# Kernel tuning notes

Measured on AMD Instinct MI355X. Metric: run time of the kernel, lower is better.

The kernel has to match this reference:

```python
import jax, jax.numpy as jnp
import numpy as np

B, T, C = 4, 2048, 2048
N_HEAD = 16
HEAD_DIM = C // N_HEAD  # 128


def _apply_rotary_emb(x, cos, sin):
    # x: (B, T, H, D), cos/sin: (1, T, 1, D/2)
    d = x.shape[-1] // 2
    x1, x2 = x[..., :d], x[..., d:]
    return jnp.concatenate([x1 * cos + x2 * sin, -x2 * sin + x1 * cos], axis=-1)


def setup_inputs() -> dict:
    key = jax.random.key(0)
    ks = jax.random.split(key, 7)
    s = 0.02
    return {
        "x": jax.random.normal(ks[0], (B, T, C), dtype=jnp.float32),
        "cos": jax.random.normal(ks[1], (1, T, 1, HEAD_DIM // 2), dtype=jnp.float32),
        "sin": jax.random.normal(ks[2], (1, T, 1, HEAD_DIM // 2), dtype=jnp.float32),
        "wq": jax.random.normal(ks[3], (C, C), dtype=jnp.float32) * s,
        "wk": jax.random.normal(ks[4], (C, C), dtype=jnp.float32) * s,
        "wv": jax.random.normal(ks[5], (C, C), dtype=jnp.float32) * s,
        "wo": jax.random.normal(ks[6], (C, C), dtype=jnp.float32) * s,
    }


def reference(x, cos, sin, wq, wk, wv, wo):
    b, t, c = x.shape
    h, d = N_HEAD, HEAD_DIM
    # linear projections (torch Linear: x @ W.T), reshape to (B, T, H, D)
    q = (x @ wq.T).reshape(b, t, h, d)
    k = (x @ wk.T).reshape(b, t, h, d)
    v = (x @ wv.T).reshape(b, t, h, d)
    q = _apply_rotary_emb(q, cos, sin)
    k = _apply_rotary_emb(k, cos, sin)
    # scaled dot-product attention, non-causal; heads on axis 2
    scale = 1.0 / jnp.sqrt(jnp.float32(d))
    scores = jnp.einsum("bqhd,bkhd->bhqk", q, k) * scale
    attn = jax.nn.softmax(scores, axis=-1)
    y = jnp.einsum("bhqk,bkhd->bqhd", attn, v).reshape(b, t, c)
    return y @ wo.T
```

## Files before the change

### kernel.cpp

```cpp
#include <hip/hip_runtime.h>

#define B_SZ 4
#define T_SZ 2048
#define C_SZ 2048
#define H_SZ 16
#define D_SZ 128

typedef __attribute__((ext_vector_type(8))) __bf16 bf16x8;
typedef __attribute__((ext_vector_type(4))) float f32x4;
typedef __attribute__((ext_vector_type(4))) unsigned short us4;

static __device__ __forceinline__ unsigned short f2bf(float f) {
  unsigned u = __builtin_bit_cast(unsigned, f);
  u += 0x7fffu + ((u >> 16) & 1u);
  return (unsigned short)(u >> 16);
}

static __device__ __forceinline__ void gload16(const void* g, void* l) {
  __builtin_amdgcn_global_load_lds((__attribute__((address_space(1))) void*)(g),
                                   (__attribute__((address_space(3))) void*)(l), 16, 0, 0);
}

__global__ __launch_bounds__(256) void cast_f32_bf16(const float* __restrict__ src,
                                                     unsigned short* __restrict__ dst, int n4) {
  int i = blockIdx.x * 256 + threadIdx.x;
  if (i >= n4) return;
  float4 v = ((const float4*)src)[i];
  us4 o;
  o[0] = f2bf(v.x); o[1] = f2bf(v.y); o[2] = f2bf(v.z); o[3] = f2bf(v.w);
  ((us4*)dst)[i] = o;
}

template <int EPI>
__global__ __launch_bounds__(256) void gemm_bt(const unsigned short* __restrict__ A,
                                               const unsigned short* __restrict__ W,
                                               void* __restrict__ out,
                                               const float* __restrict__ cosp,
                                               const float* __restrict__ sinp,
                                               float outScale, int M, int N, int K) {
  __shared__ unsigned short As[128 * 32];
  __shared__ unsigned short Bs[128 * 32];
  const int tid = threadIdx.x;
  const int wave = tid >> 6, lane = tid & 63, quad = lane >> 4, l15 = lane & 15;
  const int m0 = blockIdx.y * 128, n0 = blockIdx.x * 128;
  f32x4 acc[2][8] = {};
  for (int kt = 0; kt < K; kt += 32) {
    __syncthreads();
#pragma unroll
    for (int s = 0; s < 2; ++s) {
      int i = s * 256 + tid;
      int row = i >> 2, pos = i & 3, c = pos ^ (row & 3);
      gload16(A + (size_t)(m0 + row) * K + kt + c * 8, (char*)As + i * 16);
      gload16(W + (size_t)(n0 + row) * K + kt + c * 8, (char*)Bs + i * 16);
    }
    __syncthreads();
    const int sw = (quad ^ (l15 & 3)) * 8;
    bf16x8 a0 = *(const bf16x8*)&As[(wave * 32 + l15) * 32 + sw];
    bf16x8 a1 = *(const bf16x8*)&As[(wave * 32 + 16 + l15) * 32 + sw];
#pragma unroll
    for (int nt = 0; nt < 8; ++nt) {
      bf16x8 b = *(const bf16x8*)&Bs[(nt * 16 + l15) * 32 + sw];
      acc[0][nt] = __builtin_amdgcn_mfma_f32_16x16x32_bf16(a0, b, acc[0][nt], 0, 0, 0);
      acc[1][nt] = __builtin_amdgcn_mfma_f32_16x16x32_bf16(a1, b, acc[1][nt], 0, 0, 0);
    }
  }
  const int mb = m0 + wave * 32;
  if (EPI == 1) {
    unsigned short* O = (unsigned short*)out;
#pragma unroll
    for (int mt = 0; mt < 2; ++mt)
#pragma unroll
      for (int r = 0; r < 4; ++r) {
        int m = mb + mt * 16 + quad * 4 + r;
        int t = m & (T_SZ - 1);
#pragma unroll
        for (int nt = 0; nt < 4; ++nt) {
          int dd = nt * 16 + l15;
          float c = cosp[t * 64 + dd];
          float s = sinp[t * 64 + dd];
          float x1 = acc[mt][nt][r], x2 = acc[mt][nt + 4][r];
          O[(size_t)m * N + n0 + dd]      = f2bf((x1 * c + x2 * s) * outScale);
          O[(size_t)m * N + n0 + dd + 64] = f2bf((x1 * c - x2 * s) * outScale);
        }
      }
  } else if (EPI == 2) {
    unsigned short* O = (unsigned short*)out;
#pragma unroll
    for (int mt = 0; mt < 2; ++mt) {
      int m4 = mb + mt * 16 + quad * 4;
      int bb = m4 >> 11;
      int t = m4 & (T_SZ - 1);
#pragma unroll
      for (int nt = 0; nt < 8; ++nt) {
        int n = n0 + nt * 16 + l15;
        int h = n >> 7, d = n & (D_SZ - 1);
        us4 pk;
        pk[0] = f2bf(acc[mt][nt][0]);
        pk[1] = f2bf(acc[mt][nt][1]);
        pk[2] = f2bf(acc[mt][nt][2]);
        pk[3] = f2bf(acc[mt][nt][3]);
        *(us4*)&O[((size_t)((bb * H_SZ + h) * D_SZ + d)) * T_SZ + t] = pk;
      }
    }
  } else {
    float* O = (float*)out;
#pragma unroll
    for (int mt = 0; mt < 2; ++mt)
#pragma unroll
      for (int nt = 0; nt < 8; ++nt)
#pragma unroll
        for (int r = 0; r < 4; ++r) {
          int m = mb + mt * 16 + quad * 4 + r;
          O[(size_t)m * N + n0 + nt * 16 + l15] = acc[mt][nt][r];
        }
  }
}

__global__ __launch_bounds__(256, 2) void attn_fused(const unsigned short* __restrict__ Q,
                                                     const unsigned short* __restrict__ Kg,
                                                     const unsigned short* __restrict__ Vt,
                                                     unsigned short* __restrict__ Y) {
  __shared__ unsigned short Ks[2][64 * 128];
  __shared__ unsigned short Vs[2][128 * 64];
  __shared__ unsigned short Ps[4][32 * 40];
  const int tid = threadIdx.x;
  const int wave = tid >> 6, lane = tid & 63, quad = lane >> 4, l15 = lane & 15;
  const int kh = wave & 1, qh = wave >> 1;
  const int qt = blockIdx.x, bh = blockIdx.y;
  const int b = bh >> 4, h = bh & 15;
  const float LOG2E = 1.44269504088896f;

  bf16x8 aq[2][4];
  {
    size_t qrow0 = (size_t)(b * T_SZ + qt * 64 + qh * 32);
#pragma unroll
    for (int nt = 0; nt < 2; ++nt)
#pragma unroll
      for (int ks = 0; ks < 4; ++ks)
        aq[nt][ks] = *(const bf16x8*)(Q + (qrow0 + nt * 16 + l15) * C_SZ + h * D_SZ + ks * 32 + quad * 8);
  }

  const size_t kbase0 = ((size_t)(b * T_SZ)) * C_SZ + h * D_SZ;
  const size_t vbase0 = ((size_t)(bh * D_SZ)) * T_SZ;
#pragma unroll
  for (int s = 0; s < 4; ++s) {
    int ii = s * 256 + tid;
    int krow = ii >> 4, kpos = ii & 15, kc = kpos ^ (krow & 15);
    gload16(Kg + kbase0 + (size_t)krow * C_SZ + kc * 8, (char*)Ks[0] + ii * 16);
    int vrow = ii >> 3, vpos = ii & 7, vc = vpos ^ (vrow & 7);
    gload16(Vt + vbase0 + (size_t)vrow * T_SZ + vc * 8, (char*)Vs[0] + ii * 16);
  }
  float mstate[2] = {-1e30f, -1e30f}, lstate[2] = {0.f, 0.f};
  f32x4 o[8][2] = {};
  unsigned short* PsW = Ps[wave];
  __syncthreads();

  for (int kt = 0; kt < T_SZ / 64; ++kt) {
    const int cur = kt & 1;
    bf16x8 bk[2][4];
#pragma unroll
    for (int mt = 0; mt < 2; ++mt)
#pragma unroll
      for (int ks = 0; ks < 4; ++ks)
        bk[mt][ks] = *(const bf16x8*)&Ks[cur][(kh * 32 + mt * 16 + l15) * 128 + (((ks * 4 + quad) ^ l15) * 8)];
    bf16x8 bv[8];
#pragma unroll
    for (int dt = 0; dt < 8; ++dt)
      bv[dt] = *(const bf16x8*)&Vs[cur][(dt * 16 + l15) * 64 + (((kh * 4 + quad) ^ (l15 & 7)) * 8)];
    if (kt + 1 < T_SZ / 64) {
      const int nxt = cur ^ 1;
      size_t kb = kbase0 + (size_t)(kt + 1) * 64 * C_SZ;
      size_t vb = vbase0 + (size_t)(kt + 1) * 64;
#pragma unroll
      for (int s = 0; s < 4; ++s) {
        int ii = s * 256 + tid;
        int krow = ii >> 4, kpos = ii & 15, kc = kpos ^ (krow & 15);
        gload16(Kg + kb + (size_t)krow * C_SZ + kc * 8, (char*)Ks[nxt] + ii * 16);
        int vrow = ii >> 3, vpos = ii & 7, vc = vpos ^ (vrow & 7);
        gload16(Vt + vb + (size_t)vrow * T_SZ + vc * 8, (char*)Vs[nxt] + ii * 16);
      }
    }
    f32x4 sf[2][2] = {};
#pragma unroll
    for (int mt = 0; mt < 2; ++mt)
#pragma unroll
      for (int ks = 0; ks < 4; ++ks)
#pragma unroll
        for (int nt = 0; nt < 2; ++nt)
          sf[mt][nt] = __builtin_amdgcn_mfma_f32_16x16x32_bf16(bk[mt][ks], aq[nt][ks], sf[mt][nt], 0, 0, 0);
    float alpha[2];
#pragma unroll
    for (int nt = 0; nt < 2; ++nt) {
      float rmax = sf[0][nt][0];
#pragma unroll
      for (int mt = 0; mt < 2; ++mt)
#pragma unroll
        for (int r = 0; r < 4; ++r) rmax = fmaxf(rmax, sf[mt][nt][r]);
      rmax = fmaxf(rmax, __shfl_xor(rmax, 16));
      rmax = fmaxf(rmax, __shfl_xor(rmax, 32));
      float mnew = fmaxf(mstate[nt], rmax);
      alpha[nt] = exp2f((mstate[nt] - mnew) * LOG2E);
      float rsum = 0.f;
#pragma unroll
      for (int mt = 0; mt < 2; ++mt) {
        us4 pk;
#pragma unroll
        for (int r = 0; r < 4; ++r) {
          float p = exp2f((sf[mt][nt][r] - mnew) * LOG2E);
          rsum += p;
          pk[r] = f2bf(p);
        }
        *(us4*)&PsW[(nt * 16 + l15) * 40 + mt * 16 + quad * 4] = pk;
      }
      rsum += __shfl_xor(rsum, 16);
      rsum += __shfl_xor(rsum, 32);
      lstate[nt] = lstate[nt] * alpha[nt] + rsum;
      mstate[nt] = mnew;
    }
#pragma unroll
    for (int dt = 0; dt < 8; ++dt)
#pragma unroll
      for (int nt = 0; nt < 2; ++nt)
#pragma unroll
        for (int r = 0; r < 4; ++r) o[dt][nt][r] *= alpha[nt];
    bf16x8 ap[2];
#pragma unroll
    for (int nt = 0; nt < 2; ++nt)
      ap[nt] = *(const bf16x8*)&PsW[(nt * 16 + l15) * 40 + quad * 8];
#pragma unroll
    for (int dt = 0; dt < 8; ++dt)
#pragma unroll
      for (int nt = 0; nt < 2; ++nt)
        o[dt][nt] = __builtin_amdgcn_mfma_f32_16x16x32_bf16(bv[dt], ap[nt], o[dt][nt], 0, 0, 0);
    __syncthreads();
  }

  float* Xch = (float*)Ks;
  float* st  = (float*)Vs;
  if (kh == 1) {
#pragma unroll
    for (int dt = 0; dt < 8; ++dt)
#pragma unroll
      for (int nt = 0; nt < 2; ++nt)
        *(f32x4*)&Xch[((qh * 16 + dt * 2 + nt) * 64 + lane) * 4] = o[dt][nt];
    if (quad == 0) {
#pragma unroll
      for (int nt = 0; nt < 2; ++nt) {
        int q = qh * 32 + nt * 16 + l15;
        st[q] = mstate[nt];
        st[64 + q] = lstate[nt];
      }
    }
  }
  __syncthreads();
  if (kh == 0) {
#pragma unroll
    for (int nt = 0; nt < 2; ++nt) {
      int q = qh * 32 + nt * 16 + l15;
      float m1 = st[q], l1 = st[64 + q];
      float M = fmaxf(mstate[nt], m1);
      float a0 = exp2f((mstate[nt] - M) * LOG2E);
      float a1 = exp2f((m1 - M) * LOG2E);
      float L = lstate[nt] * a0 + l1 * a1;
      float inv = 1.0f / L;
      size_t row = (size_t)(b * T_SZ + qt * 64) + q;
#pragma unroll
      for (int dt = 0; dt < 8; ++dt) {
        f32x4 o1 = *(const f32x4*)&Xch[((qh * 16 + dt * 2 + nt) * 64 + lane) * 4];
        us4 pk;
#pragma unroll
        for (int r = 0; r < 4; ++r)
          pk[r] = f2bf((o[dt][nt][r] * a0 + o1[r] * a1) * inv);
        *(us4*)&Y[row * C_SZ + h * D_SZ + dt * 16 + quad * 4] = pk;
      }
    }
  }
}

extern "C" void kernel_launch(void* const* d_in, const int* in_sizes, int n_in,
                              void* d_out, int out_size, void* d_ws, size_t ws_size,
                              hipStream_t stream) {
  (void)in_sizes; (void)n_in; (void)out_size; (void)ws_size;
  const float* x    = (const float*)d_in[0];
  const float* cosp = (const float*)d_in[1];
  const float* sinp = (const float*)d_in[2];
  const float* wq   = (const float*)d_in[3];
  const float* wk   = (const float*)d_in[4];
  const float* wv   = (const float*)d_in[5];
  const float* wo   = (const float*)d_in[6];
  float* out = (float*)d_out;

  const size_t XE = (size_t)B_SZ * T_SZ * C_SZ;
  const size_t WE = (size_t)C_SZ * C_SZ;
  unsigned short* Xb = (unsigned short*)d_ws;
  unsigned short* Qb = Xb + XE;
  unsigned short* Kb = Qb + XE;
  unsigned short* Vt = Kb + XE;
  unsigned short* Wb = Vt + XE;
  unsigned short* Y  = Xb;

  const int M = B_SZ * T_SZ, N = C_SZ, K = C_SZ;
  dim3 ggrid(N / 128, M / 128);
  int nbx = (int)(XE / 4 / 256);
  int nbw = (int)(WE / 4 / 256);
  const float qscale = 0.088388347648318447f;

  cast_f32_bf16<<<nbx, 256, 0, stream>>>(x, Xb, (int)(XE / 4));

  cast_f32_bf16<<<nbw, 256, 0, stream>>>(wq, Wb, (int)(WE / 4));
  gemm_bt<1><<<ggrid, 256, 0, stream>>>(Xb, Wb, Qb, cosp, sinp, qscale, M, N, K);

  cast_f32_bf16<<<nbw, 256, 0, stream>>>(wk, Wb, (int)(WE / 4));
  gemm_bt<1><<<ggrid, 256, 0, stream>>>(Xb, Wb, Kb, cosp, sinp, 1.0f, M, N, K);

  cast_f32_bf16<<<nbw, 256, 0, stream>>>(wv, Wb, (int)(WE / 4));
  gemm_bt<2><<<ggrid, 256, 0, stream>>>(Xb, Wb, Vt, nullptr, nullptr, 1.0f, M, N, K);

  attn_fused<<<dim3(T_SZ / 64, B_SZ * H_SZ), 256, 0, stream>>>(Qb, Kb, Vt, Y);

  cast_f32_bf16<<<nbw, 256, 0, stream>>>(wo, Wb, (int)(WE / 4));
  gemm_bt<3><<<ggrid, 256, 0, stream>>>(Y, Wb, out, nullptr, nullptr, 1.0f, M, N, K);
}
```

Baseline: 871.9 us.

## Process two KV tiles per iteration with a single shared online-softmax rescale

The attention loop now handles two 64-key tiles per iteration. It computes both score blocks, takes one running max over 128 keys, and rescales the output accumulator once per pair instead of once per tile. Refills of each LDS buffer are issued as soon as that buffer has been read, behind a barrier, instead of prefetching one tile ahead. This halves the rescale and max-reduction overhead and moves the barriers around. In exchange it raises register pressure (two sets of K/V fragments and score tiles held live), which could hurt occupancy at the launch bound of 2 blocks.

```diff
diff --git a/kernel.cpp b/kernel.cpp
--- a/kernel.cpp
+++ b/kernel.cpp
@@ -116,6 +116,22 @@
   }
 }
 
+static __device__ __forceinline__ void stage_kv(const unsigned short* __restrict__ Kg,
+                                                const unsigned short* __restrict__ Vt,
+                                                unsigned short* Kbuf, unsigned short* Vbuf,
+                                                size_t kbase0, size_t vbase0, int kt, int tid) {
+  size_t kb = kbase0 + (size_t)kt * 64 * C_SZ;
+  size_t vb = vbase0 + (size_t)kt * 64;
+#pragma unroll
+  for (int s = 0; s < 4; ++s) {
+    int ii = s * 256 + tid;
+    int krow = ii >> 4, kpos = ii & 15, kc = kpos ^ (krow & 15);
+    gload16(Kg + kb + (size_t)krow * C_SZ + kc * 8, (char*)Kbuf + ii * 16);
+    int vrow = ii >> 3, vpos = ii & 7, vc = vpos ^ (vrow & 7);
+    gload16(Vt + vb + (size_t)vrow * T_SZ + vc * 8, (char*)Vbuf + ii * 16);
+  }
+}
+
 __global__ __launch_bounds__(256, 2) void attn_fused(const unsigned short* __restrict__ Q,
                                                      const unsigned short* __restrict__ Kg,
                                                      const unsigned short* __restrict__ Vt,
@@ -142,97 +158,131 @@
 
   const size_t kbase0 = ((size_t)(b * T_SZ)) * C_SZ + h * D_SZ;
   const size_t vbase0 = ((size_t)(bh * D_SZ)) * T_SZ;
-#pragma unroll
-  for (int s = 0; s < 4; ++s) {
-    int ii = s * 256 + tid;
-    int krow = ii >> 4, kpos = ii & 15, kc = kpos ^ (krow & 15);
-    gload16(Kg + kbase0 + (size_t)krow * C_SZ + kc * 8, (char*)Ks[0] + ii * 16);
-    int vrow = ii >> 3, vpos = ii & 7, vc = vpos ^ (vrow & 7);
-    gload16(Vt + vbase0 + (size_t)vrow * T_SZ + vc * 8, (char*)Vs[0] + ii * 16);
-  }
+  stage_kv(Kg, Vt, Ks[0], Vs[0], kbase0, vbase0, 0, tid);
+  stage_kv(Kg, Vt, Ks[1], Vs[1], kbase0, vbase0, 1, tid);
+
   float mstate[2] = {-1e30f, -1e30f}, lstate[2] = {0.f, 0.f};
   f32x4 o[8][2] = {};
   unsigned short* PsW = Ps[wave];
   __syncthreads();
 
-  for (int kt = 0; kt < T_SZ / 64; ++kt) {
-    const int cur = kt & 1;
-    bf16x8 bk[2][4];
-#pragma unroll
-    for (int mt = 0; mt < 2; ++mt)
-#pragma unroll
-      for (int ks = 0; ks < 4; ++ks)
-        bk[mt][ks] = *(const bf16x8*)&Ks[cur][(kh * 32 + mt * 16 + l15) * 128 + (((ks * 4 + quad) ^ l15) * 8)];
-    bf16x8 bv[8];
+  for (int jt = 0; jt < T_SZ / 128; ++jt) {
+    bf16x8 bkA[2][4], bvA[8];
+#pragma unroll
+    for (int mt = 0; mt < 2; ++mt)
+#pragma unroll
+      for (int ks = 0; ks < 4; ++ks)
+        bkA[mt][ks] = *(const bf16x8*)&Ks[0][(kh * 32 + mt * 16 + l15) * 128 + (((ks * 4 + quad) ^ l15) * 8)];
 #pragma unroll
     for (int dt = 0; dt < 8; ++dt)
-      bv[dt] = *(const bf16x8*)&Vs[cur][(dt * 16 + l15) * 64 + (((kh * 4 + quad) ^ (l15 & 7)) * 8)];
-    if (kt + 1 < T_SZ / 64) {
-      const int nxt = cur ^ 1;
-      size_t kb = kbase0 + (size_t)(kt + 1) * 64 * C_SZ;
-      size_t vb = vbase0 + (size_t)(kt + 1) * 64;
-#pragma unroll
-      for (int s = 0; s < 4; ++s) {
-        int ii = s * 256 + tid;
-        int krow = ii >> 4, kpos = ii & 15, kc = kpos ^ (krow & 15);
-        gload16(Kg + kb + (size_t)krow * C_SZ + kc * 8, (char*)Ks[nxt] + ii * 16);
-        int vrow = ii >> 3, vpos = ii & 7, vc = vpos ^ (vrow & 7);
-        gload16(Vt + vb + (size_t)vrow * T_SZ + vc * 8, (char*)Vs[nxt] + ii * 16);
-      }
-    }
-    f32x4 sf[2][2] = {};
+      bvA[dt] = *(const bf16x8*)&Vs[0][(dt * 16 + l15) * 64 + (((kh * 4 + quad) ^ (l15 & 7)) * 8)];
+    f32x4 sfA[2][2] = {};
 #pragma unroll
     for (int mt = 0; mt < 2; ++mt)
 #pragma unroll
       for (int ks = 0; ks < 4; ++ks)
 #pragma unroll
         for (int nt = 0; nt < 2; ++nt)
-          sf[mt][nt] = __builtin_amdgcn_mfma_f32_16x16x32_bf16(bk[mt][ks], aq[nt][ks], sf[mt][nt], 0, 0, 0);
-    float alpha[2];
+          sfA[mt][nt] = __builtin_amdgcn_mfma_f32_16x16x32_bf16(bkA[mt][ks], aq[nt][ks], sfA[mt][nt], 0, 0, 0);
+    __syncthreads();
+    if (jt + 1 < T_SZ / 128) stage_kv(Kg, Vt, Ks[0], Vs[0], kbase0, vbase0, 2 * jt + 2, tid);
+    bf16x8 bkB[2][4], bvB[8];
+#pragma unroll
+    for (int mt = 0; mt < 2; ++mt)
+#pragma unroll
+      for (int ks = 0; ks < 4; ++ks)
+        bkB[mt][ks] = *(const bf16x8*)&Ks[1][(kh * 32 + mt * 16 + l15) * 128 + (((ks * 4 + quad) ^ l15) * 8)];
+#pragma unroll
+    for (int dt = 0; dt < 8; ++dt)
+      bvB[dt] = *(const bf16x8*)&Vs[1][(dt * 16 + l15) * 64 + (((kh * 4 + quad) ^ (l15 & 7)) * 8)];
+    f32x4 sfB[2][2] = {};
+#pragma unroll
+    for (int mt = 0; mt < 2; ++mt)
+#pragma unroll
+      for (int ks = 0; ks < 4; ++ks)
+#pragma unroll
+        for (int nt = 0; nt < 2; ++nt)
+          sfB[mt][nt] = __builtin_amdgcn_mfma_f32_16x16x32_bf16(bkB[mt][ks], aq[nt][ks], sfB[mt][nt], 0, 0, 0);
+    float alpha[2], rsum[2];
 #pragma unroll
     for (int nt = 0; nt < 2; ++nt) {
-      float rmax = sf[0][nt][0];
+      float rmax = sfA[0][nt][0];
 #pragma unroll
       for (int mt = 0; mt < 2; ++mt)
 #pragma unroll
-        for (int r = 0; r < 4; ++r) rmax = fmaxf(rmax, sf[mt][nt][r]);
+        for (int r = 0; r < 4; ++r) {
+          rmax = fmaxf(rmax, sfA[mt][nt][r]);
+          rmax = fmaxf(rmax, sfB[mt][nt][r]);
+        }
       rmax = fmaxf(rmax, __shfl_xor(rmax, 16));
       rmax = fmaxf(rmax, __shfl_xor(rmax, 32));
       float mnew = fmaxf(mstate[nt], rmax);
       alpha[nt] = exp2f((mstate[nt] - mnew) * LOG2E);
-      float rsum = 0.f;
+      mstate[nt] = mnew;
+      rsum[nt] = 0.f;
+    }
+#pragma unroll
+    for (int dt = 0; dt < 8; ++dt)
+#pragma unroll
+      for (int nt = 0; nt < 2; ++nt)
+        o[dt][nt] *= alpha[nt];
+#pragma unroll
+    for (int nt = 0; nt < 2; ++nt)
 #pragma unroll
       for (int mt = 0; mt < 2; ++mt) {
         us4 pk;
-#pragma unroll
-        for (int r = 0; r < 4; ++r) {
-          float p = exp2f((sf[mt][nt][r] - mnew) * LOG2E);
-          rsum += p;
-          pk[r] = f2bf(p);
-        }
+        float p0 = exp2f((sfA[mt][nt][0] - mstate[nt]) * LOG2E);
+        float p1 = exp2f((sfA[mt][nt][1] - mstate[nt]) * LOG2E);
+        float p2 = exp2f((sfA[mt][nt][2] - mstate[nt]) * LOG2E);
+        float p3 = exp2f((sfA[mt][nt][3] - mstate[nt]) * LOG2E);
+        rsum[nt] += (p0 + p1) + (p2 + p3);
+        pk[0] = f2bf(p0); pk[1] = f2bf(p1); pk[2] = f2bf(p2); pk[3] = f2bf(p3);
         *(us4*)&PsW[(nt * 16 + l15) * 40 + mt * 16 + quad * 4] = pk;
       }
-      rsum += __shfl_xor(rsum, 16);
-      rsum += __shfl_xor(rsum, 32);
-      lstate[nt] = lstate[nt] * alpha[nt] + rsum;
-      mstate[nt] = mnew;
-    }
-#pragma unroll
-    for (int dt = 0; dt < 8; ++dt)
+    {
+      bf16x8 ap[2];
 #pragma unroll
       for (int nt = 0; nt < 2; ++nt)
-#pragma unroll
-        for (int r = 0; r < 4; ++r) o[dt][nt][r] *= alpha[nt];
-    bf16x8 ap[2];
+        ap[nt] = *(const bf16x8*)&PsW[(nt * 16 + l15) * 40 + quad * 8];
+#pragma unroll
+      for (int dt = 0; dt < 8; ++dt)
+#pragma unroll
+        for (int nt = 0; nt < 2; ++nt)
+          o[dt][nt] = __builtin_amdgcn_mfma_f32_16x16x32_bf16(bvA[dt], ap[nt], o[dt][nt], 0, 0, 0);
+    }
+    asm volatile("" ::: "memory");
 #pragma unroll
     for (int nt = 0; nt < 2; ++nt)
-      ap[nt] = *(const bf16x8*)&PsW[(nt * 16 + l15) * 40 + quad * 8];
-#pragma unroll
-    for (int dt = 0; dt < 8; ++dt)
+#pragma unroll
+      for (int mt = 0; mt < 2; ++mt) {
+        us4 pk;
+        float p0 = exp2f((sfB[mt][nt][0] - mstate[nt]) * LOG2E);
+        float p1 = exp2f((sfB[mt][nt][1] - mstate[nt]) * LOG2E);
+        float p2 = exp2f((sfB[mt][nt][2] - mstate[nt]) * LOG2E);
+        float p3 = exp2f((sfB[mt][nt][3] - mstate[nt]) * LOG2E);
+        rsum[nt] += (p0 + p1) + (p2 + p3);
+        pk[0] = f2bf(p0); pk[1] = f2bf(p1); pk[2] = f2bf(p2); pk[3] = f2bf(p3);
+        *(us4*)&PsW[(nt * 16 + l15) * 40 + mt * 16 + quad * 4] = pk;
+      }
+    {
+      bf16x8 ap[2];
 #pragma unroll
       for (int nt = 0; nt < 2; ++nt)
-        o[dt][nt] = __builtin_amdgcn_mfma_f32_16x16x32_bf16(bv[dt], ap[nt], o[dt][nt], 0, 0, 0);
+        ap[nt] = *(const bf16x8*)&PsW[(nt * 16 + l15) * 40 + quad * 8];
+#pragma unroll
+      for (int dt = 0; dt < 8; ++dt)
+#pragma unroll
+        for (int nt = 0; nt < 2; ++nt)
+          o[dt][nt] = __builtin_amdgcn_mfma_f32_16x16x32_bf16(bvB[dt], ap[nt], o[dt][nt], 0, 0, 0);
+    }
+#pragma unroll
+    for (int nt = 0; nt < 2; ++nt) {
+      rsum[nt] += __shfl_xor(rsum[nt], 16);
+      rsum[nt] += __shfl_xor(rsum[nt], 32);
+      lstate[nt] = lstate[nt] * alpha[nt] + rsum[nt];
+    }
     __syncthreads();
+    if (jt + 1 < T_SZ / 128) stage_kv(Kg, Vt, Ks[1], Vs[1], kbase0, vbase0, 2 * jt + 3, tid);
   }
 
   float* Xch = (float*)Ks;
@@ -268,9 +318,10 @@
       for (int dt = 0; dt < 8; ++dt) {
         f32x4 o1 = *(const f32x4*)&Xch[((qh * 16 + dt * 2 + nt) * 64 + lane) * 4];
         us4 pk;
-#pragma unroll
-        for (int r = 0; r < 4; ++r)
-          pk[r] = f2bf((o[dt][nt][r] * a0 + o1[r] * a1) * inv);
+        pk[0] = f2bf((o[dt][nt][0] * a0 + o1[0] * a1) * inv);
+        pk[1] = f2bf((o[dt][nt][1] * a0 + o1[1] * a1) * inv);
+        pk[2] = f2bf((o[dt][nt][2] * a0 + o1[2] * a1) * inv);
+        pk[3] = f2bf((o[dt][nt][3] * a0 + o1[3] * a1) * inv);
         *(us4*)&Y[row * C_SZ + h * D_SZ + dt * 16 + quad * 4] = pk;
       }
     }
```

Result: faster. 850.2 us (-2.5%).
